# Performance work log

Measured on AMD Instinct MI355X. Metric: run time of the kernel, lower is better.

Reference implementation:

```python
import jax, jax.numpy as jnp
import numpy as np

B, N, F = 8, 2048, 32  # batch, num_nodes, out_features
AVG_DEG = 32


def setup_inputs() -> dict:
    key = jax.random.key(0)
    k1, k2, k3, k4 = jax.random.split(key, 4)
    x = jax.random.normal(k1, (B, N, N + 1), dtype=jnp.float32)
    # kaiming-uniform-ish scale for weight, small uniform for bias
    bound_w = 1.0 / np.sqrt(N + 1)
    weight = jax.random.uniform(k2, (N, N + 1, F), jnp.float32, -bound_w, bound_w)
    bound_b = 1.0 / np.sqrt((N + 1) * F)
    bias = jax.random.uniform(k3, (N, F), jnp.float32, -bound_b, bound_b)
    # random symmetric adjacency with self-loops, avg degree ~AVG_DEG
    adj = jax.random.bernoulli(k4, AVG_DEG / N, (N, N))
    adj = adj | adj.T | jnp.eye(N, dtype=bool)
    # prepend an always-kept column (the ones column in the torch code)
    keep = jnp.concatenate([jnp.ones((N, 1), dtype=bool), adj], axis=1)  # [N, N+1]
    edge_mask = ~keep  # True = zero out (masked_fill semantics)
    return {"x": x, "weight": weight, "bias": bias, "edge_mask": edge_mask}


def reference(x, weight, bias, edge_mask):
    # mask: zero non-neighbor entries per node (broadcast over batch)
    xm = jnp.where(edge_mask[None, :, :], jnp.float32(0.0), x)  # [B, N, N+1]
    # per-node batched matmul: [B,N,N+1] x [N,N+1,F] -> [B,N,F]
    out = jnp.einsum('bnk,nkf->bnf', xm, weight)
    return out + bias[None, :, :]
```

## Files before the change

kernel.cpp:

```cpp
#include <hip/hip_runtime.h>


constexpr int NB = 8;
constexpr int NN = 2048;
constexpr int NK = 2049;
constexpr int NF = 32;

template <int MODE>
__device__ __forceinline__ void kloop(const float* __restrict__ x,
                                      const float* __restrict__ wrow,
                                      const void* __restrict__ mask,
                                      int n, int fq, int klane,
                                      float acc[NB][4]) {
  const size_t xstride = (size_t)NN * NK;
  const float* xn = x + (size_t)n * NK;
  const int mbase = n * NK;

  for (int t = 0; t < 17; ++t) {
    const int kb = t * 128 + klane;
    float4 wv[4];
    float sc[4];
    float xv[4][NB];
#pragma unroll
    for (int u = 0; u < 4; ++u) {
      const int ku = kb + u * 32;
      const int kc = (ku < NK) ? ku : (NK - 1);
      const bool valid = (ku < NK);
      bool keep;
      if (MODE == 0)
        keep = (((const int*)mask)[mbase + kc] == 0);
      else if (MODE == 1)
        keep = (((const unsigned char*)mask)[mbase + kc] == 0);
      else
        keep = (((const float*)mask)[mbase + kc] == 0.0f);
      sc[u] = (valid && keep) ? 1.0f : 0.0f;
      wv[u] = *(const float4*)(wrow + (size_t)kc * NF + fq * 4);
#pragma unroll
      for (int b = 0; b < NB; ++b)
        xv[u][b] = xn[(size_t)b * xstride + kc];
    }
#pragma unroll
    for (int u = 0; u < 4; ++u) {
      float4 wm;
      wm.x = wv[u].x * sc[u];
      wm.y = wv[u].y * sc[u];
      wm.z = wv[u].z * sc[u];
      wm.w = wv[u].w * sc[u];
#pragma unroll
      for (int b = 0; b < NB; ++b) {
        acc[b][0] = fmaf(xv[u][b], wm.x, acc[b][0]);
        acc[b][1] = fmaf(xv[u][b], wm.y, acc[b][1]);
        acc[b][2] = fmaf(xv[u][b], wm.z, acc[b][2]);
        acc[b][3] = fmaf(xv[u][b], wm.w, acc[b][3]);
      }
    }
  }
}

__global__ __launch_bounds__(256) void snl_kernel(
    const float* __restrict__ x, const float* __restrict__ w,
    const float* __restrict__ bias, const void* __restrict__ mask,
    float* __restrict__ out) {
  __shared__ float part[4][8][32];
  __shared__ int smode;

  const int tid = threadIdx.x;
  const int n = blockIdx.x;

  if (tid < 64) {
    unsigned v = ((const unsigned*)mask)[tid];
    unsigned long long bf = __ballot((v >> 24) == 0x3Fu);
    unsigned long long bg = __ballot(v > 1u);
    if (tid == 0) smode = bf ? 2 : (bg ? 1 : 0);
  }
  __syncthreads();
  const int mode = smode;

  const int fq = tid & 7;
  const int kk = (tid >> 3) & 7;
  const int ws = tid >> 6;
  const int klane = ws * 8 + kk;

  float acc[NB][4];
#pragma unroll
  for (int b = 0; b < NB; ++b)
#pragma unroll
    for (int j = 0; j < 4; ++j) acc[b][j] = 0.0f;

  const float* wrow = w + (size_t)n * NK * NF;

  if (mode == 1)
    kloop<1>(x, wrow, mask, n, fq, klane, acc);
  else if (mode == 0)
    kloop<0>(x, wrow, mask, n, fq, klane, acc);
  else
    kloop<2>(x, wrow, mask, n, fq, klane, acc);

#pragma unroll
  for (int m = 8; m <= 32; m <<= 1) {
#pragma unroll
    for (int b = 0; b < NB; ++b)
#pragma unroll
      for (int j = 0; j < 4; ++j)
        acc[b][j] += __shfl_xor(acc[b][j], m, 64);
  }
  if ((tid & 63) < 8) {
#pragma unroll
    for (int b = 0; b < NB; ++b)
#pragma unroll
      for (int j = 0; j < 4; ++j) part[ws][fq][b * 4 + j] = acc[b][j];
  }
  __syncthreads();

  if (tid < 64) {
    const int b = tid >> 3;
    const int f2 = tid & 7;
    float4 o = *(const float4*)(bias + n * NF + f2 * 4);
#pragma unroll
    for (int wsi = 0; wsi < 4; ++wsi) {
      const float4 p = *(const float4*)&part[wsi][f2][b * 4];
      o.x += p.x;
      o.y += p.y;
      o.z += p.z;
      o.w += p.w;
    }
    *(float4*)(out + ((size_t)b * NN + n) * NF + f2 * 4) = o;
  }
}

extern "C" void kernel_launch(void* const* d_in, const int* in_sizes, int n_in,
                              void* d_out, int out_size, void* d_ws,
                              size_t ws_size, hipStream_t stream) {
  const float* x = (const float*)d_in[0];
  const float* w = (const float*)d_in[1];
  const float* bias = (const float*)d_in[2];
  const void* mask = d_in[3];
  float* out = (float*)d_out;

  hipLaunchKernelGGL(snl_kernel, dim3(NN), dim3(256), 0, stream, x, w, bias,
                     mask, out);
}
```

Baseline: 136.5 us.

## Stage masked x tiles through double-buffered LDS with coalesced loads

Result: no change. 134.4 us (-1.6%).

```diff
diff --git a/kernel.cpp b/kernel.cpp
--- a/kernel.cpp
+++ b/kernel.cpp
@@ -5,62 +5,25 @@
 constexpr int NN = 2048;
 constexpr int NK = 2049;
 constexpr int NF = 32;
+constexpr size_t XSTR = (size_t)NN * NK;
 
-template <int MODE>
-__device__ __forceinline__ void kloop(const float* __restrict__ x,
-                                      const float* __restrict__ wrow,
-                                      const void* __restrict__ mask,
-                                      int n, int fq, int klane,
-                                      float acc[NB][4]) {
-  const size_t xstride = (size_t)NN * NK;
-  const float* xn = x + (size_t)n * NK;
-  const int mbase = n * NK;
-
-  for (int t = 0; t < 17; ++t) {
-    const int kb = t * 128 + klane;
-    float4 wv[4];
-    float sc[4];
-    float xv[4][NB];
-#pragma unroll
-    for (int u = 0; u < 4; ++u) {
-      const int ku = kb + u * 32;
-      const int kc = (ku < NK) ? ku : (NK - 1);
-      const bool valid = (ku < NK);
-      bool keep;
-      if (MODE == 0)
-        keep = (((const int*)mask)[mbase + kc] == 0);
-      else if (MODE == 1)
-        keep = (((const unsigned char*)mask)[mbase + kc] == 0);
-      else
-        keep = (((const float*)mask)[mbase + kc] == 0.0f);
-      sc[u] = (valid && keep) ? 1.0f : 0.0f;
-      wv[u] = *(const float4*)(wrow + (size_t)kc * NF + fq * 4);
-#pragma unroll
-      for (int b = 0; b < NB; ++b)
-        xv[u][b] = xn[(size_t)b * xstride + kc];
-    }
-#pragma unroll
-    for (int u = 0; u < 4; ++u) {
-      float4 wm;
-      wm.x = wv[u].x * sc[u];
-      wm.y = wv[u].y * sc[u];
-      wm.z = wv[u].z * sc[u];
-      wm.w = wv[u].w * sc[u];
-#pragma unroll
-      for (int b = 0; b < NB; ++b) {
-        acc[b][0] = fmaf(xv[u][b], wm.x, acc[b][0]);
-        acc[b][1] = fmaf(xv[u][b], wm.y, acc[b][1]);
-        acc[b][2] = fmaf(xv[u][b], wm.z, acc[b][2]);
-        acc[b][3] = fmaf(xv[u][b], wm.w, acc[b][3]);
-      }
-    }
-  }
+__device__ __forceinline__ float ld_scale(const void* __restrict__ mask,
+                                          size_t idx, int mode) {
+  bool drop;
+  if (mode == 0)
+    drop = ((const int*)mask)[idx] != 0;
+  else if (mode == 1)
+    drop = ((const unsigned char*)mask)[idx] != 0;
+  else
+    drop = ((const float*)mask)[idx] != 0.0f;
+  return drop ? 0.0f : 1.0f;
 }
 
 __global__ __launch_bounds__(256) void snl_kernel(
     const float* __restrict__ x, const float* __restrict__ w,
     const float* __restrict__ bias, const void* __restrict__ mask,
     float* __restrict__ out) {
+  __shared__ float xs[2][NB][128];
   __shared__ float part[4][8][32];
   __shared__ int smode;
 
@@ -81,20 +44,61 @@
   const int ws = tid >> 6;
   const int klane = ws * 8 + kk;
 
+  const int sk = tid & 127;
+  const int sh = tid >> 7;
+
+  const float* xn = x + (size_t)n * NK;
+  const float* wrow = w + (size_t)n * NK * NF;
+  const size_t mbase = (size_t)n * NK;
+
   float acc[NB][4];
 #pragma unroll
   for (int b = 0; b < NB; ++b)
 #pragma unroll
     for (int j = 0; j < 4; ++j) acc[b][j] = 0.0f;
 
-  const float* wrow = w + (size_t)n * NK * NF;
+  {
+    const float sc = ld_scale(mask, mbase + sk, mode);
+#pragma unroll
+    for (int i = 0; i < 4; ++i)
+      xs[0][sh * 4 + i][sk] = xn[(size_t)(sh * 4 + i) * XSTR + sk] * sc;
+  }
+  __syncthreads();
 
-  if (mode == 1)
-    kloop<1>(x, wrow, mask, n, fq, klane, acc);
-  else if (mode == 0)
-    kloop<0>(x, wrow, mask, n, fq, klane, acc);
-  else
-    kloop<2>(x, wrow, mask, n, fq, klane, acc);
+  for (int t = 0; t < 16; ++t) {
+    const int cur = t & 1;
+    const bool pf = (t + 1 < 16);
+    float xr[4], scr = 0.0f;
+    if (pf) {
+      const int kg = (t + 1) * 128 + sk;
+      scr = ld_scale(mask, mbase + kg, mode);
+#pragma unroll
+      for (int i = 0; i < 4; ++i)
+        xr[i] = xn[(size_t)(sh * 4 + i) * XSTR + kg];
+    }
+
+    const float* wt = wrow + (size_t)t * 128 * NF;
+#pragma unroll
+    for (int u = 0; u < 4; ++u) {
+      const int kl = u * 32 + klane;
+      const float4 wv = *(const float4*)(wt + (size_t)kl * NF + fq * 4);
+#pragma unroll
+      for (int b = 0; b < NB; ++b) {
+        const float xv = xs[cur][b][kl];
+        acc[b][0] = fmaf(xv, wv.x, acc[b][0]);
+        acc[b][1] = fmaf(xv, wv.y, acc[b][1]);
+        acc[b][2] = fmaf(xv, wv.z, acc[b][2]);
+        acc[b][3] = fmaf(xv, wv.w, acc[b][3]);
+      }
+    }
+
+    if (pf) {
+#pragma unroll
+      for (int i = 0; i < 4; ++i)
+        xs[cur ^ 1][sh * 4 + i][sk] = xr[i] * scr;
+    }
+    __syncthreads();
+  }
 
 #pragma unroll
   for (int m = 8; m <= 32; m <<= 1) {
@@ -115,7 +119,16 @@
   if (tid < 64) {
     const int b = tid >> 3;
     const int f2 = tid & 7;
-    float4 o = *(const float4*)(bias + n * NF + f2 * 4);
+    float4 o = *(const float4*)(bias + (size_t)n * NF + f2 * 4);
+    {
+      const float sc = ld_scale(mask, mbase + 2048, mode);
+      const float xv = xn[(size_t)b * XSTR + 2048] * sc;
+      const float4 wv = *(const float4*)(wrow + (size_t)2048 * NF + f2 * 4);
+      o.x += xv * wv.x;
+      o.y += xv * wv.y;
+      o.z += xv * wv.z;
+      o.w += xv * wv.w;
+    }
 #pragma unroll
     for (int wsi = 0; wsi < 4; ++wsi) {
       const float4 p = *(const float4*)&part[wsi][f2][b * 4];
```
